# Optimization experiments

Measured on AMD Instinct MI355X. Metric: run time of the kernel, lower is better.

## Reference

```python
import jax, jax.numpy as jnp
import numpy as np

GENE_DIM = 3008   # conf.gene_dim
H = 6             # conf.num_hiddens_genotype (per-term hidden dim)
D_MODEL = 768     # conf.d_model
B = 4096          # batch
SIZES = [2048, 512, 128, 32, 8, 1]   # terms per topological layer (leaves -> root)
GPL = 8           # direct genes per leaf term
EPS = 1e-5        # BatchNorm1d eps


def setup_inputs() -> dict:
    key = jax.random.key(0)
    keys = iter(jax.random.split(key, 64))

    def rn(shape, scale=0.05):
        return jax.random.normal(next(keys), shape, dtype=jnp.float32) * scale

    inp = {"x": jax.random.normal(next(keys), (B, GENE_DIM), dtype=jnp.float32)}
    # batched per-leaf direct_gene_layer: Linear(GENE_DIM, GPL) for each leaf term
    inp["Wg"] = rn((SIZES[0], GPL, GENE_DIM))
    inp["bg"] = rn((SIZES[0], GPL))
    # per-layer term linear + batchnorm params; input sizes per layer
    in_sizes = [GPL, 4 * H, 4 * H, 4 * H, 4 * H, 8 * H]
    for i, (t, c) in enumerate(zip(SIZES, in_sizes)):
        inp[f"W{i}"] = rn((t, H, c))
        inp[f"b{i}"] = rn((t, H))
        inp[f"gm{i}"] = jnp.ones((t, H), jnp.float32)
        inp[f"bt{i}"] = jnp.zeros((t, H), jnp.float32)
    inp["Wf"] = rn((D_MODEL, H))
    inp["bf"] = rn((D_MODEL,))
    return inp


def _term_layer(child, W, b, gm, bt):
    # child: [B, T, in] ; W: [T, H, in] -> per-term Linear + tanh + BatchNorm1d(train)
    h = jnp.tanh(jnp.einsum('bti,toi->bto', child, W) + b)
    mu = h.mean(axis=0)              # [T, H] batch stats (biased var, as torch BN)
    var = h.var(axis=0)
    return (h - mu) * jax.lax.rsqrt(var + EPS) * gm + bt


def reference(x, Wg, bg,
              W0, b0, gm0, bt0, W1, b1, gm1, bt1, W2, b2, gm2, bt2,
              W3, b3, gm3, bt3, W4, b4, gm4, bt4, W5, b5, gm5, bt5,
              Wf, bf):
    gene = x[:, :GENE_DIM].astype(jnp.float32)        # x.narrow(1, 0, gene_dim)
    # all leaf direct_gene_layers batched: [B, T0, GPL]
    g = jnp.einsum('bg,tog->bto', gene, Wg) + bg
    h = _term_layer(g, W0, b0, gm0, bt0)              # leaf term layer: [B, T0, H]
    layer_params = [(W1, b1, gm1, bt1), (W2, b2, gm2, bt2), (W3, b3, gm3, bt3),
                    (W4, b4, gm4, bt4), (W5, b5, gm5, bt5)]
    for (W, b, gm, bt), T in zip(layer_params, SIZES[1:]):
        # gather-concat of child term outputs: contiguous fanout blocks -> reshape
        child = h.reshape(h.shape[0], T, -1)          # [B, T, fanout*H]
        h = _term_layer(child, W, b, gm, bt)
    root = h[:, 0, :]                                 # [B, H]
    return root @ Wf.T + bf                           # final_linear_layer -> [B, D_MODEL]
```

## Files before the change

### kernel.cpp

```cpp
#include <hip/hip_runtime.h>


typedef float f32x4 __attribute__((ext_vector_type(4)));
typedef __bf16 bf16x8 __attribute__((ext_vector_type(8)));

#define GL2LDS(g, l)                                                          \
  __builtin_amdgcn_global_load_lds(                                           \
      (__attribute__((address_space(1))) void*)(g),                           \
      (__attribute__((address_space(3))) void*)(l), 16, 0, 0)

__device__ __forceinline__ unsigned short f2bf(float f) {
  unsigned int u = __float_as_uint(f);
  u = u + 0x7fffu + ((u >> 16) & 1u);
  return (unsigned short)(u >> 16);
}

__device__ __forceinline__ float bf2f(unsigned int lo16) {
  return __uint_as_float(lo16 << 16);
}

__device__ __forceinline__ float tanh_fast(float x) {
  float e = __expf(2.0f * x);
  return 1.0f - __fdividef(2.0f, e + 1.0f);
}

__global__ __launch_bounds__(256) void cvt_all(
    const float* __restrict__ x, const float* __restrict__ wg,
    unsigned short* __restrict__ xb, unsigned short* __restrict__ wgb) {
  constexpr int NX = 12320768 / 4;
  constexpr int NW = 49283072 / 4;
  int i = blockIdx.x * 256 + threadIdx.x;
  const float* src;
  unsigned short* dst;
  int j;
  if (i < NX) {
    src = x; dst = xb; j = i;
  } else {
    j = i - NX;
    if (j >= NW) return;
    src = wg; dst = wgb;
  }
  float4 v = ((const float4*)src)[j];
  ushort4 o;
  o.x = f2bf(v.x); o.y = f2bf(v.y); o.z = f2bf(v.z); o.w = f2bf(v.w);
  ((ushort4*)dst)[j] = o;
}

__global__ __launch_bounds__(512, 2) void gemm_bt(
    const unsigned short* __restrict__ A, const unsigned short* __restrict__ Bm,
    const float* __restrict__ bias, unsigned short* __restrict__ C) {
  constexpr int N = 16384, K = 3008;
  __shared__ unsigned short lds[65536];
  const int tid = threadIdx.x;
  const int w = tid >> 6, l = tid & 63;
  const int m0 = blockIdx.y * 256, n0 = blockIdx.x * 256;

  const int r0 = tid >> 3;
  const int c0 = (tid & 7) ^ (r0 & 7);
  const unsigned short* gA = A + (size_t)(m0 + r0) * K + c0 * 8;
  const unsigned short* gB = Bm + (size_t)(n0 + r0) * K + c0 * 8;
  const int wbase = w * 512;

#define ASLOT(par, h) (lds + ((((par) << 1) | (h)) * 8192))
#define BSLOT(par, h) (lds + 32768 + ((((par) << 1) | (h)) * 8192))

#define STAGEA(par, h, kofE)                                                  \
  do {                                                                        \
    unsigned short* d_ = ASLOT(par, h) + wbase;                               \
    GL2LDS(gA + (size_t)((h) * 128) * K + (kofE), d_);                        \
    GL2LDS(gA + (size_t)((h) * 128 + 64) * K + (kofE), d_ + 4096);            \
  } while (0)
#define STAGEB(par, h, kofE)                                                  \
  do {                                                                        \
    unsigned short* d_ = BSLOT(par, h) + wbase;                               \
    GL2LDS(gB + (size_t)((h) * 128) * K + (kofE), d_);                        \
    GL2LDS(gB + (size_t)((h) * 128 + 64) * K + (kofE), d_ + 4096);            \
  } while (0)

  const int quad = l >> 4, lrow = l & 15;
  int aO[2][4], bO[2][2];
#pragma unroll
  for (int f = 0; f < 4; ++f) {
    int ra = (w >> 2) * 64 + f * 16 + lrow;
#pragma unroll
    for (int kk = 0; kk < 2; ++kk)
      aO[kk][f] = ra * 64 + (((kk * 4 + quad) ^ (ra & 7)) * 8);
  }
#pragma unroll
  for (int n = 0; n < 2; ++n) {
    int rb = (w & 3) * 32 + n * 16 + lrow;
#pragma unroll
    for (int kk = 0; kk < 2; ++kk)
      bO[kk][n] = rb * 64 + (((kk * 4 + quad) ^ (rb & 7)) * 8);
  }

  f32x4 acc[8][4];
#pragma unroll
  for (int i = 0; i < 8; ++i)
#pragma unroll
    for (int j = 0; j < 4; ++j) acc[i][j] = (f32x4)0.0f;
  bf16x8 av[4][2], bv[2][2];

#define VM4 asm volatile("s_waitcnt vmcnt(4)" ::: "memory")
#define VM0 asm volatile("s_waitcnt vmcnt(0)" ::: "memory")
#define NOVM ((void)0)

#define PHASE(par, mh, nh, LA, LB, STG, VMSTMT)                               \
  {                                                                           \
    if (LA) {                                                                 \
      _Pragma("unroll") for (int f = 0; f < 4; ++f) {                         \
        av[f][0] = *(const bf16x8*)(ASLOT(par, mh) + aO[0][f]);               \
        av[f][1] = *(const bf16x8*)(ASLOT(par, mh) + aO[1][f]);               \
      }                                                                       \
    }                                                                         \
    if (LB) {                                                                 \
      _Pragma("unroll") for (int n = 0; n < 2; ++n) {                         \
        bv[n][0] = *(const bf16x8*)(BSLOT(par, nh) + bO[0][n]);               \
        bv[n][1] = *(const bf16x8*)(BSLOT(par, nh) + bO[1][n]);               \
      }                                                                       \
    }                                                                         \
    STG;                                                                      \
    VMSTMT;                                                                   \
    __builtin_amdgcn_s_barrier();                                             \
    asm volatile("s_waitcnt lgkmcnt(0)" ::: "memory");                        \
    __builtin_amdgcn_sched_barrier(0);                                        \
    __builtin_amdgcn_s_setprio(1);                                            \
    _Pragma("unroll") for (int f = 0; f < 4; ++f)                             \
      _Pragma("unroll") for (int n = 0; n < 2; ++n) {                         \
        acc[(mh) * 4 + f][(nh) * 2 + n] =                                     \
            __builtin_amdgcn_mfma_f32_16x16x32_bf16(                          \
                av[f][0], bv[n][0], acc[(mh) * 4 + f][(nh) * 2 + n], 0, 0, 0);\
        acc[(mh) * 4 + f][(nh) * 2 + n] =                                     \
            __builtin_amdgcn_mfma_f32_16x16x32_bf16(                          \
                av[f][1], bv[n][1], acc[(mh) * 4 + f][(nh) * 2 + n], 0, 0, 0);\
      }                                                                       \
    __builtin_amdgcn_s_setprio(0);                                            \
    __builtin_amdgcn_s_barrier();                                             \
  }

#define STEP(par, S1, S2, VMSTMT)                                             \
  PHASE(par, 0, 0, true, true, if (S1) STAGEA((par) ^ 1, 0, kof + 64), NOVM); \
  PHASE(par, 1, 0, true, false, if (S1) STAGEB((par) ^ 1, 1, kof + 64), NOVM);\
  PHASE(par, 1, 1, false, true, if (S2) STAGEB(par, 0, kof + 128), NOVM);     \
  PHASE(par, 0, 1, true, false, if (S2) STAGEA(par, 1, kof + 128), VMSTMT);   \
  kof += 64;

  int kof = 0;
  STAGEA(0, 0, 0); STAGEB(0, 0, 0); STAGEA(0, 1, 0); STAGEB(0, 1, 0);
  STAGEB(1, 0, 64); STAGEA(1, 1, 64);
  VM4;
  __builtin_amdgcn_s_barrier();

  for (int it = 0; it < 22; ++it) {
    STEP(0, true, true, VM4);
    STEP(1, true, true, VM4);
  }
  STEP(0, true, true, VM4);
  STEP(1, true, false, VM0);
  STEP(0, false, false, NOVM);

#undef STEP
#undef PHASE
#undef STAGEA
#undef STAGEB
#undef ASLOT
#undef BSLOT

#pragma unroll
  for (int bn = 0; bn < 4; ++bn) {
    int n = n0 + (bn >> 1) * 128 + (w & 3) * 32 + (bn & 1) * 16 + lrow;
    float bnv = bias[n];
#pragma unroll
    for (int F = 0; F < 8; ++F) {
      int mbase = m0 + (F >> 2) * 128 + (w >> 2) * 64 + (F & 3) * 16 + quad * 4;
#pragma unroll
      for (int r = 0; r < 4; ++r) {
        C[(size_t)(mbase + r) * N + n] = f2bf(acc[F][bn][r] + bnv);
      }
    }
  }
}

template <int IC>
__device__ __forceinline__ void load_row(const unsigned short* p, float* d) {
  static_assert(IC % 8 == 0, "");
#pragma unroll
  for (int i = 0; i < IC / 8; ++i) {
    uint4 u = *(const uint4*)(p + i * 8);
    d[i * 8 + 0] = bf2f(u.x & 0xffffu); d[i * 8 + 1] = bf2f(u.x >> 16);
    d[i * 8 + 2] = bf2f(u.y & 0xffffu); d[i * 8 + 3] = bf2f(u.y >> 16);
    d[i * 8 + 4] = bf2f(u.z & 0xffffu); d[i * 8 + 5] = bf2f(u.z >> 16);
    d[i * 8 + 6] = bf2f(u.w & 0xffffu); d[i * 8 + 7] = bf2f(u.w >> 16);
  }
}
template <int IC>
__device__ __forceinline__ void load_row(const float* p, float* d) {
  static_assert(IC % 4 == 0, "");
#pragma unroll
  for (int i = 0; i < IC / 4; ++i) {
    float4 v = *(const float4*)(p + i * 4);
    d[i * 4 + 0] = v.x; d[i * 4 + 1] = v.y;
    d[i * 4 + 2] = v.z; d[i * 4 + 3] = v.w;
  }
}

template <typename TIN, typename TOUT, int T, int IC, int TG, bool FIRST>
__global__ __launch_bounds__(256) void term_layer(
    const TIN* __restrict__ in, const float* __restrict__ prevStats,
    const float* __restrict__ prevGm, const float* __restrict__ prevBt,
    const float* __restrict__ W, const float* __restrict__ bvec,
    TOUT* __restrict__ out, float* __restrict__ curStats) {
  constexpr int WIN = T * IC;
  constexpr int WOUT = T * 6;
  constexpr int NB = 256 / TG;
  const int tb = blockIdx.x * TG;
  const int t = threadIdx.x & (TG - 1);
  const int bsub = threadIdx.x / TG;

  __shared__ float sW[TG * 6 * IC];
  __shared__ float sB[TG * 6];
  __shared__ float sScale[FIRST ? 1 : TG * IC];
  __shared__ float sShift[FIRST ? 1 : TG * IC];
  __shared__ float sRed[256][13];

  for (int i = threadIdx.x; i < TG * 6 * IC; i += 256)
    sW[i] = W[(size_t)tb * 6 * IC + i];
  for (int i = threadIdx.x; i < TG * 6; i += 256) sB[i] = bvec[tb * 6 + i];
  if constexpr (!FIRST) {
    for (int i = threadIdx.x; i < TG * IC; i += 256) {
      int gc = tb * IC + i;
      float mu = prevStats[gc] * (1.0f / 4096.0f);
      float var = prevStats[WIN + gc] * (1.0f / 4096.0f) - mu * mu;
      float sc = rsqrtf(var + 1e-5f) * prevGm[gc];
      sScale[i] = sc;
      sShift[i] = prevBt[gc] - mu * sc;
    }
  }
  __syncthreads();

  float ls[6], lq[6];
#pragma unroll
  for (int i = 0; i < 6; ++i) { ls[i] = 0.0f; lq[i] = 0.0f; }

  const int bchunk = 4096 / gridDim.y;
  const int rows = bchunk / NB;
  const int b0 = blockIdx.y * bchunk + bsub * rows;
  for (int i = 0; i < rows; ++i) {
    int b = b0 + i;
    float child[IC];
    load_row<IC>(in + (size_t)b * WIN + (size_t)(tb + t) * IC, child);
    if constexpr (!FIRST) {
#pragma unroll
      for (int c = 0; c < IC; ++c)
        child[c] = child[c] * sScale[t * IC + c] + sShift[t * IC + c];
    }
    float hv[6];
#pragma unroll
    for (int o = 0; o < 6; ++o) {
      float a = sB[t * 6 + o];
      const float* wr = &sW[(t * 6 + o) * IC];
#pragma unroll
      for (int j = 0; j < IC; ++j) a += child[j] * wr[j];
      float h = tanh_fast(a);
      hv[o] = h;
      ls[o] += h;
      lq[o] += h * h;
    }
    TOUT* op = out + (size_t)b * WOUT + (size_t)(tb + t) * 6;
    if constexpr (sizeof(TOUT) == 2) {
      unsigned int* oi = (unsigned int*)op;
#pragma unroll
      for (int i2 = 0; i2 < 3; ++i2)
        oi[i2] = (unsigned int)f2bf(hv[2 * i2]) |
                 ((unsigned int)f2bf(hv[2 * i2 + 1]) << 16);
    } else {
#pragma unroll
      for (int i2 = 0; i2 < 6; ++i2) op[i2] = hv[i2];
    }
  }

#pragma unroll
  for (int j = 0; j < 6; ++j) {
    sRed[threadIdx.x][j] = ls[j];
    sRed[threadIdx.x][6 + j] = lq[j];
  }
  __syncthreads();
  for (int i = threadIdx.x; i < TG * 6; i += 256) {
    int tt = i / 6, o = i % 6;
    float s = 0.0f, q = 0.0f;
    for (int nb = 0; nb < NB; ++nb) {
      s += sRed[nb * TG + tt][o];
      q += sRed[nb * TG + tt][6 + o];
    }
    atomicAdd(&curStats[(tb + tt) * 6 + o], s);
    atomicAdd(&curStats[WOUT + (tb + tt) * 6 + o], q);
  }
}

__global__ __launch_bounds__(256) void final_fc(
    const float* __restrict__ h5, const float* __restrict__ stats5,
    const float* __restrict__ gm5, const float* __restrict__ bt5,
    const float* __restrict__ Wf, const float* __restrict__ bfv,
    float* __restrict__ out) {
  __shared__ float sWf[768 * 6];
  __shared__ float sbf[768];
  __shared__ float sRoot[8][6];
  const int tid = threadIdx.x;
  for (int i = tid; i < 768 * 6; i += 256) sWf[i] = Wf[i];
  for (int i = tid; i < 768; i += 256) sbf[i] = bfv[i];
  const int b0 = blockIdx.x * 8;
  if (tid < 48) {
    int bb = tid / 6, o = tid % 6;
    float mu = stats5[o] * (1.0f / 4096.0f);
    float var = stats5[6 + o] * (1.0f / 4096.0f) - mu * mu;
    float sc = rsqrtf(var + 1e-5f) * gm5[o];
    sRoot[bb][o] = (h5[(size_t)(b0 + bb) * 6 + o] - mu) * sc + bt5[o];
  }
  __syncthreads();
#pragma unroll
  for (int bb = 0; bb < 8; ++bb) {
    float r0 = sRoot[bb][0], r1 = sRoot[bb][1], r2 = sRoot[bb][2];
    float r3 = sRoot[bb][3], r4 = sRoot[bb][4], r5 = sRoot[bb][5];
    for (int d = tid; d < 768; d += 256) {
      const float* wr = &sWf[d * 6];
      float a = sbf[d] + r0 * wr[0] + r1 * wr[1] + r2 * wr[2] +
                r3 * wr[3] + r4 * wr[4] + r5 * wr[5];
      out[(size_t)(b0 + bb) * 768 + d] = a;
    }
  }
}

extern "C" void kernel_launch(void* const* d_in, const int* in_sizes, int n_in,
                              void* d_out, int out_size, void* d_ws,
                              size_t ws_size, hipStream_t stream) {
  const float* x   = (const float*)d_in[0];
  const float* Wg  = (const float*)d_in[1];
  const float* bg  = (const float*)d_in[2];
  const float* W0  = (const float*)d_in[3];
  const float* b0v = (const float*)d_in[4];
  const float* gm0 = (const float*)d_in[5];
  const float* bt0 = (const float*)d_in[6];
  const float* W1  = (const float*)d_in[7];
  const float* b1v = (const float*)d_in[8];
  const float* gm1 = (const float*)d_in[9];
  const float* bt1 = (const float*)d_in[10];
  const float* W2  = (const float*)d_in[11];
  const float* b2v = (const float*)d_in[12];
  const float* gm2 = (const float*)d_in[13];
  const float* bt2 = (const float*)d_in[14];
  const float* W3  = (const float*)d_in[15];
  const float* b3v = (const float*)d_in[16];
  const float* gm3 = (const float*)d_in[17];
  const float* bt3 = (const float*)d_in[18];
  const float* W4  = (const float*)d_in[19];
  const float* b4v = (const float*)d_in[20];
  const float* gm4 = (const float*)d_in[21];
  const float* bt4 = (const float*)d_in[22];
  const float* W5  = (const float*)d_in[23];
  const float* b5v = (const float*)d_in[24];
  const float* gm5 = (const float*)d_in[25];
  const float* bt5 = (const float*)d_in[26];
  const float* Wf  = (const float*)d_in[27];
  const float* bfv = (const float*)d_in[28];

  char* ws = (char*)d_ws;
  unsigned short* Xb  = (unsigned short*)(ws + 0);
  unsigned short* Wgb = (unsigned short*)(ws + 24641536ULL);
  unsigned short* G   = (unsigned short*)(ws + 123207680ULL);
  unsigned short* h0  = (unsigned short*)(ws + 257425408ULL);
  unsigned short* h1  = (unsigned short*)(ws + 358088704ULL);
  unsigned short* h2  = (unsigned short*)(ws + 383254528ULL);
  float* h3 = (float*)(ws + 389545984ULL);
  float* h4 = (float*)(ws + 392691712ULL);
  float* h5 = (float*)(ws + 393478144ULL);
  float* stats = (float*)(ws + 393576448ULL);

  hipMemsetAsync(stats, 0, 131072, stream);

  cvt_all<<<dim3(60160), 256, 0, stream>>>(x, Wg, Xb, Wgb);

  gemm_bt<<<dim3(64, 16), 512, 0, stream>>>(Xb, Wgb, bg, G);

  term_layer<unsigned short, unsigned short, 2048, 8, 64, true>
      <<<dim3(32, 64), 256, 0, stream>>>(G, nullptr, nullptr, nullptr, W0, b0v,
                                         h0, stats + 0);
  term_layer<unsigned short, unsigned short, 512, 24, 32, false>
      <<<dim3(16, 64), 256, 0, stream>>>(h0, stats + 0, gm0, bt0, W1, b1v, h1,
                                         stats + 24576);
  term_layer<unsigned short, unsigned short, 128, 24, 32, false>
      <<<dim3(4, 128), 256, 0, stream>>>(h1, stats + 24576, gm1, bt1, W2, b2v,
                                         h2, stats + 30720);
  term_layer<unsigned short, float, 32, 24, 32, false>
      <<<dim3(1, 128), 256, 0, stream>>>(h2, stats + 30720, gm2, bt2, W3, b3v,
                                         h3, stats + 32256);
  term_layer<float, float, 8, 24, 8, false>
      <<<dim3(1, 64), 256, 0, stream>>>(h3, stats + 32256, gm3, bt3, W4, b4v,
                                        h4, stats + 32640);
  term_layer<float, float, 1, 48, 1, false>
      <<<dim3(1, 16), 256, 0, stream>>>(h4, stats + 32640, gm4, bt4, W5, b5v,
                                        h5, stats + 32736);

  final_fc<<<dim3(512), 256, 0, stream>>>(h5, stats + 32736, gm5, bt5, Wf, bfv,
                                          (float*)d_out);
}
```

Baseline: 852.7 us.

## Restructure bf16 GEMM warp tiling to 64x128 and simplify double-buffered pipeline

Changes the per-wave tile from 128x64 split into four quadrant phases to a 64x128 tile (4 M-frags by 8 N-frags), with A fragments loaded once per k-step and B reloaded per phase. The B staging is rewritten so each wave group loads its own 128-row half of B, and the pipeline becomes a simple two-slot double buffer with a full vmcnt(0) wait at the end of each step instead of the staggered vmcnt(4) scheme. This aims to reduce LDS reads per MFMA and simplify scheduling. The full wait per step may expose more global-load latency than the previous staggered prefetch.

Result: slower. 904.0 us (+6.0%).

```diff
diff --git a/kernel.cpp b/kernel.cpp
--- a/kernel.cpp
+++ b/kernel.cpp
@@ -55,128 +55,134 @@
   const int w = tid >> 6, l = tid & 63;
   const int m0 = blockIdx.y * 256, n0 = blockIdx.x * 256;
 
+  const int quad = l >> 4, lrow = l & 15;
+  const int wm = (w >> 1) * 64;
+  const int ah = w >> 2;
+  const int bg = w & 1;
+  const int wn = bg * 128;
+
+#define ASLOT(par, h) (lds + (((par) * 2 + (h)) * 8192))
+#define BSLOT(par, h) (lds + 32768 + (((par) * 2 + (h)) * 8192))
+
   const int r0 = tid >> 3;
   const int c0 = (tid & 7) ^ (r0 & 7);
   const unsigned short* gA = A + (size_t)(m0 + r0) * K + c0 * 8;
-  const unsigned short* gB = Bm + (size_t)(n0 + r0) * K + c0 * 8;
-  const int wbase = w * 512;
-
-#define ASLOT(par, h) (lds + ((((par) << 1) | (h)) * 8192))
-#define BSLOT(par, h) (lds + 32768 + ((((par) << 1) | (h)) * 8192))
+  const int wg = w >> 1;
+  const int brl = l >> 3;
+  const int bcl = (l & 7) ^ brl;
+  const unsigned short* gBs =
+      Bm + (size_t)(n0 + bg * 128 + wg * 32 + brl) * K + bcl * 8;
+  const int bDst = wg * 2048;
 
 #define STAGEA(par, h, kofE)                                                  \
   do {                                                                        \
-    unsigned short* d_ = ASLOT(par, h) + wbase;                               \
+    unsigned short* d_ = ASLOT(par, h) + w * 512;                             \
     GL2LDS(gA + (size_t)((h) * 128) * K + (kofE), d_);                        \
     GL2LDS(gA + (size_t)((h) * 128 + 64) * K + (kofE), d_ + 4096);            \
   } while (0)
-#define STAGEB(par, h, kofE)                                                  \
+#define STAGEB2(par, j0, kofE)                                                \
   do {                                                                        \
-    unsigned short* d_ = BSLOT(par, h) + wbase;                               \
-    GL2LDS(gB + (size_t)((h) * 128) * K + (kofE), d_);                        \
-    GL2LDS(gB + (size_t)((h) * 128 + 64) * K + (kofE), d_ + 4096);            \
+    unsigned short* d_ = BSLOT(par, bg) + bDst + (j0) * 512;                  \
+    GL2LDS(gBs + (size_t)((j0) * 8) * K + (kofE), d_);                        \
+    GL2LDS(gBs + (size_t)((j0) * 8 + 8) * K + (kofE), d_ + 512);              \
   } while (0)
 
-  const int quad = l >> 4, lrow = l & 15;
-  int aO[2][4], bO[2][2];
-#pragma unroll
-  for (int f = 0; f < 4; ++f) {
-    int ra = (w >> 2) * 64 + f * 16 + lrow;
+  int aOff[2][4], bOff[2][4];
+#pragma unroll
+  for (int m = 0; m < 4; ++m) {
+    int rh = (wm & 127) + m * 16 + lrow;
 #pragma unroll
     for (int kk = 0; kk < 2; ++kk)
-      aO[kk][f] = ra * 64 + (((kk * 4 + quad) ^ (ra & 7)) * 8);
-  }
-#pragma unroll
-  for (int n = 0; n < 2; ++n) {
-    int rb = (w & 3) * 32 + n * 16 + lrow;
+      aOff[kk][m] = rh * 64 + (((kk * 4 + quad) ^ (lrow & 7)) * 8);
+  }
+#pragma unroll
+  for (int n = 0; n < 4; ++n) {
+    int rh = n * 16 + lrow;
 #pragma unroll
     for (int kk = 0; kk < 2; ++kk)
-      bO[kk][n] = rb * 64 + (((kk * 4 + quad) ^ (rb & 7)) * 8);
-  }
-
-  f32x4 acc[8][4];
-#pragma unroll
-  for (int i = 0; i < 8; ++i)
-#pragma unroll
-    for (int j = 0; j < 4; ++j) acc[i][j] = (f32x4)0.0f;
-  bf16x8 av[4][2], bv[2][2];
-
-#define VM4 asm volatile("s_waitcnt vmcnt(4)" ::: "memory")
+      bOff[kk][n] = rh * 64 + (((kk * 4 + quad) ^ (lrow & 7)) * 8);
+  }
+
+  f32x4 acc[4][8];
+#pragma unroll
+  for (int i = 0; i < 4; ++i)
+#pragma unroll
+    for (int j = 0; j < 8; ++j) acc[i][j] = (f32x4)0.0f;
+  bf16x8 av[4][2], bv[4];
+
 #define VM0 asm volatile("s_waitcnt vmcnt(0)" ::: "memory")
 #define NOVM ((void)0)
-
-#define PHASE(par, mh, nh, LA, LB, STG, VMSTMT)                               \
+#define NOSTG ((void)0)
+
+#define PHASE(par, q, kk, LA, STG, VMAFTER)                                   \
   {                                                                           \
     if (LA) {                                                                 \
-      _Pragma("unroll") for (int f = 0; f < 4; ++f) {                         \
-        av[f][0] = *(const bf16x8*)(ASLOT(par, mh) + aO[0][f]);               \
-        av[f][1] = *(const bf16x8*)(ASLOT(par, mh) + aO[1][f]);               \
-      }                                                                       \
+      _Pragma("unroll") for (int m = 0; m < 4; ++m)                           \
+          av[m][kk] = *(const bf16x8*)(ASLOT(par, ah) + aOff[kk][m]);         \
     }                                                                         \
-    if (LB) {                                                                 \
-      _Pragma("unroll") for (int n = 0; n < 2; ++n) {                         \
-        bv[n][0] = *(const bf16x8*)(BSLOT(par, nh) + bO[0][n]);               \
-        bv[n][1] = *(const bf16x8*)(BSLOT(par, nh) + bO[1][n]);               \
-      }                                                                       \
-    }                                                                         \
+    _Pragma("unroll") for (int n = 0; n < 4; ++n)                             \
+        bv[n] = *(const bf16x8*)(BSLOT(par, bg) + bOff[kk][n] + (q) * 4096);  \
     STG;                                                                      \
-    VMSTMT;                                                                   \
     __builtin_amdgcn_s_barrier();                                             \
     asm volatile("s_waitcnt lgkmcnt(0)" ::: "memory");                        \
     __builtin_amdgcn_sched_barrier(0);                                        \
     __builtin_amdgcn_s_setprio(1);                                            \
-    _Pragma("unroll") for (int f = 0; f < 4; ++f)                             \
-      _Pragma("unroll") for (int n = 0; n < 2; ++n) {                         \
-        acc[(mh) * 4 + f][(nh) * 2 + n] =                                     \
-            __builtin_amdgcn_mfma_f32_16x16x32_bf16(                          \
-                av[f][0], bv[n][0], acc[(mh) * 4 + f][(nh) * 2 + n], 0, 0, 0);\
-        acc[(mh) * 4 + f][(nh) * 2 + n] =                                     \
-            __builtin_amdgcn_mfma_f32_16x16x32_bf16(                          \
-                av[f][1], bv[n][1], acc[(mh) * 4 + f][(nh) * 2 + n], 0, 0, 0);\
-      }                                                                       \
+    _Pragma("unroll") for (int m = 0; m < 4; ++m)                             \
+      _Pragma("unroll") for (int n = 0; n < 4; ++n)                           \
+          acc[m][(q) * 4 + n] = __builtin_amdgcn_mfma_f32_16x16x32_bf16(      \
+              av[m][kk], bv[n], acc[m][(q) * 4 + n], 0, 0, 0);                \
     __builtin_amdgcn_s_setprio(0);                                            \
+    VMAFTER;                                                                  \
+    __builtin_amdgcn_sched_barrier(0);                                        \
     __builtin_amdgcn_s_barrier();                                             \
   }
 
-#define STEP(par, S1, S2, VMSTMT)                                             \
-  PHASE(par, 0, 0, true, true, if (S1) STAGEA((par) ^ 1, 0, kof + 64), NOVM); \
-  PHASE(par, 1, 0, true, false, if (S1) STAGEB((par) ^ 1, 1, kof + 64), NOVM);\
-  PHASE(par, 1, 1, false, true, if (S2) STAGEB(par, 0, kof + 128), NOVM);     \
-  PHASE(par, 0, 1, true, false, if (S2) STAGEA(par, 1, kof + 128), VMSTMT);   \
+#define FULLSTEP(par)                                                         \
+  PHASE(par, 0, 0, true, NOSTG, NOVM);                                        \
+  PHASE(par, 0, 1, true,                                                      \
+        STAGEA((par) ^ 1, 0, kof + 64); STAGEB2((par) ^ 1, 0, kof + 64),      \
+        NOVM);                                                                \
+  PHASE(par, 1, 0, false,                                                     \
+        STAGEA((par) ^ 1, 1, kof + 64); STAGEB2((par) ^ 1, 2, kof + 64),      \
+        NOVM);                                                                \
+  PHASE(par, 1, 1, false, NOSTG, VM0);                                        \
   kof += 64;
 
+#define LASTSTEP(par)                                                         \
+  PHASE(par, 0, 0, true, NOSTG, NOVM);                                        \
+  PHASE(par, 0, 1, true, NOSTG, NOVM);                                        \
+  PHASE(par, 1, 0, false, NOSTG, NOVM);                                       \
+  PHASE(par, 1, 1, false, NOSTG, NOVM);
+
+  STAGEA(0, 0, 0); STAGEA(0, 1, 0); STAGEB2(0, 0, 0); STAGEB2(0, 2, 0);
+  VM0;
+  __builtin_amdgcn_s_barrier();
+
   int kof = 0;
-  STAGEA(0, 0, 0); STAGEB(0, 0, 0); STAGEA(0, 1, 0); STAGEB(0, 1, 0);
-  STAGEB(1, 0, 64); STAGEA(1, 1, 64);
-  VM4;
-  __builtin_amdgcn_s_barrier();
-
-  for (int it = 0; it < 22; ++it) {
-    STEP(0, true, true, VM4);
-    STEP(1, true, true, VM4);
-  }
-  STEP(0, true, true, VM4);
-  STEP(1, true, false, VM0);
-  STEP(0, false, false, NOVM);
-
-#undef STEP
+  for (int it = 0; it < 23; ++it) {
+    FULLSTEP(0);
+    FULLSTEP(1);
+  }
+  LASTSTEP(0);
+
+#undef FULLSTEP
+#undef LASTSTEP
 #undef PHASE
 #undef STAGEA
-#undef STAGEB
+#undef STAGEB2
 #undef ASLOT
 #undef BSLOT
 
 #pragma unroll
-  for (int bn = 0; bn < 4; ++bn) {
-    int n = n0 + (bn >> 1) * 128 + (w & 3) * 32 + (bn & 1) * 16 + lrow;
+  for (int nf = 0; nf < 8; ++nf) {
+    int n = n0 + wn + nf * 16 + lrow;
     float bnv = bias[n];
 #pragma unroll
-    for (int F = 0; F < 8; ++F) {
-      int mbase = m0 + (F >> 2) * 128 + (w >> 2) * 64 + (F & 3) * 16 + quad * 4;
-#pragma unroll
-      for (int r = 0; r < 4; ++r) {
-        C[(size_t)(mbase + r) * N + n] = f2bf(acc[F][bn][r] + bnv);
-      }
+    for (int m = 0; m < 4; ++m) {
+      int mbase = m0 + wm + m * 16 + quad * 4;
+#pragma unroll
+      for (int r = 0; r < 4; ++r)
+        C[(size_t)(mbase + r) * N + n] = f2bf(acc[m][nf][r] + bnv);
     }
   }
 }
```
